# Kernel tuning notes

Hardware: AMD Instinct MI355X
Metric: run time of the kernel (lower is better)

The kernel has to match this reference:

```python
import jax, jax.numpy as jnp
import numpy as np

B, N, F, C, L = 2, 2048, 64, 64, 4

def setup_inputs() -> dict:
    key = jax.random.key(0)
    k1, k2, k3, k4, k5 = jax.random.split(key, 5)
    V = jax.random.normal(k1, (B, N, F), dtype=jnp.float32)
    A = jax.random.uniform(k2, (B, N, N, L), dtype=jnp.float32)
    # xavier-normal-ish scale for w1; plain normals for w2/w3
    w1 = jax.random.normal(k3, (F, C), dtype=jnp.float32) * jnp.sqrt(2.0 / (F + C))
    w2 = jax.random.normal(k4, (F * L, C), dtype=jnp.float32) * 0.05
    w3 = jax.random.normal(k5, (F * L, C), dtype=jnp.float32) * 0.05
    return {"V": V, "A": A, "w1": w1, "w2": w2, "w3": w3}

def reference(V, A, w1, w2, w3):
    b, n, _, l = A.shape
    f = V.shape[-1]
    # term1: plain linear embedding (no bias, no act)
    term1 = jnp.matmul(V, w1)                                   # B,N,C
    # term2: per-edge-type degree weighting of self features
    deg = jnp.sum(A, axis=2)                                    # B,N,L  (sum over neighbors j)
    dv = (deg[..., None] * V[:, :, None, :]).reshape(b, n, l * f)  # B,N,L*F
    term2 = jnp.matmul(dv, w2)                                  # B,N,C
    # term3: neighbor aggregation per edge type
    agg = jnp.einsum('bijl,bjf->bilf', A, V).reshape(b, n, l * f)  # B,N,L*F
    term3 = jnp.matmul(agg, w3)                                 # B,N,C
    return jax.nn.sigmoid(term1 + term2 - term3)
```

## Files before the change

### kernel.cpp

```cpp
#include <hip/hip_runtime.h>

#define B_ 2
#define N_ 2048
#define F_ 64
#define C_ 64
#define L_ 4
#define SK 4
#define NJ (N_ / SK)
#define TSTEPS (NJ / 32)
#define PJ 40

typedef _Float16 half8 __attribute__((ext_vector_type(8)));
typedef _Float16 half2 __attribute__((ext_vector_type(2)));
typedef float floatx4 __attribute__((ext_vector_type(4)));

__global__ __launch_bounds__(256) void k0_transpose(const float* __restrict__ V,
                                                    _Float16* __restrict__ Vth) {
    __shared__ float tile[64][65];
    const int b  = blockIdx.x >> 5;
    const int j0 = (blockIdx.x & 31) * 64;
    const int tid = threadIdx.x;

    const floatx4* V4 = (const floatx4*)(V + ((size_t)(b * N_ + j0)) * F_);
#pragma unroll
    for (int s = 0; s < 4; ++s) {
        int g = tid + 256 * s;
        int jl = g >> 4;
        int fq = g & 15;
        floatx4 v = V4[jl * 16 + fq];
        tile[jl][fq * 4 + 0] = v.x;
        tile[jl][fq * 4 + 1] = v.y;
        tile[jl][fq * 4 + 2] = v.z;
        tile[jl][fq * 4 + 3] = v.w;
    }
    __syncthreads();

    const int f = tid >> 2;
    const int jb = (tid & 3) * 16;
    _Float16* dh = Vth + ((size_t)(b * F_ + f)) * N_ + j0 + jb;
#pragma unroll
    for (int u = 0; u < 16; u += 4) {
        half2 h01 = {(_Float16)tile[jb + u + 0][f], (_Float16)tile[jb + u + 1][f]};
        half2 h23 = {(_Float16)tile[jb + u + 2][f], (_Float16)tile[jb + u + 3][f]};
        *(half2*)(dh + u + 0) = h01;
        *(half2*)(dh + u + 2) = h23;
    }
}

__global__ __launch_bounds__(256, 4) void k1_agg(const float* __restrict__ A,
                                                 const _Float16* __restrict__ Vth,
                                                 float* __restrict__ aggT,
                                                 float* __restrict__ degT) {
    __shared__ _Float16 lds[2 * 4 * 16 * PJ];

    const int bid = blockIdx.x;
    const int b   = bid >> 9;
    const int rem = bid & 511;
    const int i0  = (rem >> 2) * 16;
    const int p   = rem & 3;
    const int tid  = threadIdx.x;
    const int w    = tid >> 6;
    const int lane = tid & 63;
    const int m    = lane & 15;
    const int q    = lane >> 4;

    const int i_s = tid >> 4;
    const int jp  = tid & 15;

    const floatx4* Abase = (const floatx4*)A + ((size_t)(b * N_ + i0 + i_s)) * N_ + p * NJ;
    const _Float16* Vrow = Vth + ((size_t)b * F_) * N_ + p * NJ;

    floatx4 acc0 = {0,0,0,0}, acc1 = {0,0,0,0}, acc2 = {0,0,0,0}, acc3 = {0,0,0,0};
    floatx4 accd = {0,0,0,0};

    half8 bones;
#pragma unroll
    for (int e = 0; e < 8; ++e) bones[e] = (m == 0) ? (_Float16)1.0f : (_Float16)0.0f;

    floatx4 a_cur0, a_cur1, a_nxt0, a_nxt1;
    half8 v_cur0, v_cur1, v_cur2, v_cur3, v_nxt0, v_nxt1, v_nxt2, v_nxt3;

#define LOAD_A(t, x0, x1) do { int jj = (t) * 32 + 2 * jp; x0 = Abase[jj]; x1 = Abase[jj + 1]; } while (0)
#define LOAD_V(t, v0, v1, v2, v3) do { int jj = (t) * 32 + q * 8;                                  \
        v0 = *(const half8*)(Vrow + (size_t)(0  + m) * N_ + jj);                                   \
        v1 = *(const half8*)(Vrow + (size_t)(16 + m) * N_ + jj);                                   \
        v2 = *(const half8*)(Vrow + (size_t)(32 + m) * N_ + jj);                                   \
        v3 = *(const half8*)(Vrow + (size_t)(48 + m) * N_ + jj); } while (0)

    LOAD_A(0, a_cur0, a_cur1);
    LOAD_V(0, v_cur0, v_cur1, v_cur2, v_cur3);
    LOAD_A(1, a_nxt0, a_nxt1);
    LOAD_V(1, v_nxt0, v_nxt1, v_nxt2, v_nxt3);

#pragma unroll 2
    for (int t = 0; t < TSTEPS; ++t) {
        const int buf = t & 1;
        _Float16* dst = lds + buf * (4 * 16 * PJ);
        {
            const float* c0 = (const float*)&a_cur0;
            const float* c1 = (const float*)&a_cur1;
#pragma unroll
            for (int l = 0; l < 4; ++l) {
                half2 h = {(_Float16)c0[l], (_Float16)c1[l]};
                *(half2*)(dst + (l * 16 + i_s) * PJ + 2 * jp) = h;
            }
        }
        __syncthreads();

        a_cur0 = a_nxt0; a_cur1 = a_nxt1;
        const int tn = (t + 2 < TSTEPS) ? (t + 2) : (TSTEPS - 1);
        LOAD_A(tn, a_nxt0, a_nxt1);

        half8 af = *(const half8*)(lds + buf * (4 * 16 * PJ) + (w * 16 + m) * PJ + q * 8);
        acc0 = __builtin_amdgcn_mfma_f32_16x16x32_f16(af, v_cur0, acc0, 0, 0, 0);
        acc1 = __builtin_amdgcn_mfma_f32_16x16x32_f16(af, v_cur1, acc1, 0, 0, 0);
        acc2 = __builtin_amdgcn_mfma_f32_16x16x32_f16(af, v_cur2, acc2, 0, 0, 0);
        acc3 = __builtin_amdgcn_mfma_f32_16x16x32_f16(af, v_cur3, acc3, 0, 0, 0);
        accd = __builtin_amdgcn_mfma_f32_16x16x32_f16(af, bones,  accd, 0, 0, 0);

        v_cur0 = v_nxt0; v_cur1 = v_nxt1; v_cur2 = v_nxt2; v_cur3 = v_nxt3;
        LOAD_V(tn, v_nxt0, v_nxt1, v_nxt2, v_nxt3);
    }
#undef LOAD_A
#undef LOAD_V

    float* aggb = aggT + ((size_t)(p * B_ + b)) * 256 * N_;
    const int ibase = i0 + q * 4;
    {
        int k = w * 64 + 0  + m; *(floatx4*)(aggb + (size_t)k * N_ + ibase) = acc0;
    }
    {
        int k = w * 64 + 16 + m; *(floatx4*)(aggb + (size_t)k * N_ + ibase) = acc1;
    }
    {
        int k = w * 64 + 32 + m; *(floatx4*)(aggb + (size_t)k * N_ + ibase) = acc2;
    }
    {
        int k = w * 64 + 48 + m; *(floatx4*)(aggb + (size_t)k * N_ + ibase) = acc3;
    }
    if (m == 0) {
        *(floatx4*)(degT + ((size_t)((p * B_ + b) * L_ + w)) * N_ + ibase) = accd;
    }
}

__global__ __launch_bounds__(256) void k2_out(const float* __restrict__ V,
                                              const float* __restrict__ degT,
                                              const float* __restrict__ aggT,
                                              const float* __restrict__ w1,
                                              const float* __restrict__ w2,
                                              const float* __restrict__ w3,
                                              float* __restrict__ out) {
    __shared__ float xsum[256][4];
    __shared__ float vt[4][64];
    __shared__ float dsum[4][4];

    const int raw = blockIdx.x;
    const int b   = raw >> 9;
    const int t9  = raw & 511;
    const int tile = ((t9 & 7) << 6) | (t9 >> 3);
    const int i0  = tile * 4;
    const int tid = threadIdx.x;

    {
        const int k = tid;
        const float* g = aggT + ((size_t)b * 256 + k) * N_ + i0;
        const size_t PS = (size_t)B_ * 256 * N_;
        floatx4 s = *(const floatx4*)(g);
        s += *(const floatx4*)(g + PS);
        s += *(const floatx4*)(g + 2 * PS);
        s += *(const floatx4*)(g + 3 * PS);
        *(floatx4*)&xsum[k][0] = s;
    }
    {
        const int il = tid >> 6, f = tid & 63;
        vt[il][f] = V[((size_t)(b * N_ + i0 + il)) * F_ + f];
    }
    if (tid < 16) {
        const int l = tid >> 2, il = tid & 3;
        float s = 0.0f;
#pragma unroll
        for (int p = 0; p < SK; ++p)
            s += degT[((size_t)((p * B_ + b) * L_ + l)) * N_ + i0 + il];
        dsum[l][il] = s;
    }
    __syncthreads();

    const int il = tid >> 6;
    const int c  = tid & 63;
    const float d0 = dsum[0][il], d1 = dsum[1][il], d2 = dsum[2][il], d3 = dsum[3][il];

    float acc = 0.0f;
#pragma unroll 4
    for (int f = 0; f < 64; ++f) {
        const float x = vt[il][f];
        acc += x        * w1[f * 64 + c];
        acc += (d0 * x) * w2[(0 * 64 + f) * 64 + c];
        acc += (d1 * x) * w2[(1 * 64 + f) * 64 + c];
        acc += (d2 * x) * w2[(2 * 64 + f) * 64 + c];
        acc += (d3 * x) * w2[(3 * 64 + f) * 64 + c];
    }
#pragma unroll 4
    for (int k = 0; k < 256; ++k) {
        acc -= xsum[k][il] * w3[k * 64 + c];
    }

    out[((size_t)(b * N_ + i0 + il)) * C_ + c] = 1.0f / (1.0f + __expf(-acc));
}

extern "C" void kernel_launch(void* const* d_in, const int* in_sizes, int n_in,
                              void* d_out, int out_size, void* d_ws, size_t ws_size,
                              hipStream_t stream) {
    const float* V  = (const float*)d_in[0];
    const float* A  = (const float*)d_in[1];
    const float* w1 = (const float*)d_in[2];
    const float* w2 = (const float*)d_in[3];
    const float* w3 = (const float*)d_in[4];
    float* out = (float*)d_out;

    char* ws = (char*)d_ws;
    float*    aggT = (float*)(ws);
    float*    degT = (float*)(ws + 16777216);
    _Float16* Vth  = (_Float16*)(ws + 17039360);

    hipLaunchKernelGGL(k0_transpose, dim3(B_ * (N_ / 64)), dim3(256), 0, stream, V, Vth);
    hipLaunchKernelGGL(k1_agg,       dim3(B_ * (N_ / 16) * SK), dim3(256), 0, stream,
                       A, Vth, aggT, degT);
    hipLaunchKernelGGL(k2_out,       dim3(B_ * (N_ / 4)), dim3(256), 0, stream,
                       V, degT, aggT, w1, w2, w3, out);
}
```

Baseline: 243.2 us.

## Load A directly into MFMA registers per wave, drop LDS staging, split-K by 8

```diff
diff --git a/kernel.cpp b/kernel.cpp
--- a/kernel.cpp
+++ b/kernel.cpp
@@ -5,10 +5,7 @@
 #define F_ 64
 #define C_ 64
 #define L_ 4
-#define SK 4
-#define NJ (N_ / SK)
-#define TSTEPS (NJ / 32)
-#define PJ 40
+#define SP 8
 
 typedef _Float16 half8 __attribute__((ext_vector_type(8)));
 typedef _Float16 half2 __attribute__((ext_vector_type(2)));
@@ -47,99 +44,90 @@
     }
 }
 
-__global__ __launch_bounds__(256, 4) void k1_agg(const float* __restrict__ A,
+__global__ __launch_bounds__(256, 2) void k1_agg(const float* __restrict__ A,
                                                  const _Float16* __restrict__ Vth,
                                                  float* __restrict__ aggT,
                                                  float* __restrict__ degT) {
-    __shared__ _Float16 lds[2 * 4 * 16 * PJ];
-
     const int bid = blockIdx.x;
-    const int b   = bid >> 9;
-    const int rem = bid & 511;
-    const int i0  = (rem >> 2) * 16;
-    const int p   = rem & 3;
+    const int b   = bid >> 8;
+    const int rem = bid & 255;
+    const int i0  = (rem >> 1) * 16;
+    const int h   = rem & 1;
     const int tid  = threadIdx.x;
     const int w    = tid >> 6;
     const int lane = tid & 63;
     const int m    = lane & 15;
     const int q    = lane >> 4;
-
-    const int i_s = tid >> 4;
-    const int jp  = tid & 15;
-
-    const floatx4* Abase = (const floatx4*)A + ((size_t)(b * N_ + i0 + i_s)) * N_ + p * NJ;
-    const _Float16* Vrow = Vth + ((size_t)b * F_) * N_ + p * NJ;
-
-    floatx4 acc0 = {0,0,0,0}, acc1 = {0,0,0,0}, acc2 = {0,0,0,0}, acc3 = {0,0,0,0};
-    floatx4 accd = {0,0,0,0};
+    const int p    = h * 4 + w;
+    const int jwin = p * 256;
+
+    const floatx4* Arow = (const floatx4*)(A + (((size_t)(b * N_ + i0 + m)) * N_ + jwin) * 4);
+    const _Float16* Vrow = Vth + ((size_t)b * F_) * N_ + jwin;
+
+    floatx4 acc[4][4];
+    floatx4 accd[4];
+#pragma unroll
+    for (int l = 0; l < 4; ++l) {
+        accd[l] = (floatx4){0, 0, 0, 0};
+#pragma unroll
+        for (int fc = 0; fc < 4; ++fc) acc[l][fc] = (floatx4){0, 0, 0, 0};
+    }
 
     half8 bones;
 #pragma unroll
     for (int e = 0; e < 8; ++e) bones[e] = (m == 0) ? (_Float16)1.0f : (_Float16)0.0f;
 
-    floatx4 a_cur0, a_cur1, a_nxt0, a_nxt1;
-    half8 v_cur0, v_cur1, v_cur2, v_cur3, v_nxt0, v_nxt1, v_nxt2, v_nxt3;
-
-#define LOAD_A(t, x0, x1) do { int jj = (t) * 32 + 2 * jp; x0 = Abase[jj]; x1 = Abase[jj + 1]; } while (0)
-#define LOAD_V(t, v0, v1, v2, v3) do { int jj = (t) * 32 + q * 8;                                  \
-        v0 = *(const half8*)(Vrow + (size_t)(0  + m) * N_ + jj);                                   \
-        v1 = *(const half8*)(Vrow + (size_t)(16 + m) * N_ + jj);                                   \
-        v2 = *(const half8*)(Vrow + (size_t)(32 + m) * N_ + jj);                                   \
-        v3 = *(const half8*)(Vrow + (size_t)(48 + m) * N_ + jj); } while (0)
-
-    LOAD_A(0, a_cur0, a_cur1);
-    LOAD_V(0, v_cur0, v_cur1, v_cur2, v_cur3);
-    LOAD_A(1, a_nxt0, a_nxt1);
-    LOAD_V(1, v_nxt0, v_nxt1, v_nxt2, v_nxt3);
+    half8 v_cur[4], v_nxt[4];
+#pragma unroll
+    for (int fc = 0; fc < 4; ++fc)
+        v_cur[fc] = *(const half8*)(Vrow + (size_t)(fc * 16 + m) * N_ + q * 8);
 
 #pragma unroll 2
-    for (int t = 0; t < TSTEPS; ++t) {
-        const int buf = t & 1;
-        _Float16* dst = lds + buf * (4 * 16 * PJ);
-        {
-            const float* c0 = (const float*)&a_cur0;
-            const float* c1 = (const float*)&a_cur1;
-#pragma unroll
-            for (int l = 0; l < 4; ++l) {
-                half2 h = {(_Float16)c0[l], (_Float16)c1[l]};
-                *(half2*)(dst + (l * 16 + i_s) * PJ + 2 * jp) = h;
-            }
+    for (int t = 0; t < 8; ++t) {
+        floatx4 a[8];
+        const int jb = t * 32 + q * 8;
+#pragma unroll
+        for (int e = 0; e < 8; ++e) a[e] = Arow[jb + e];
+
+        const int tn = (t < 7) ? t + 1 : 7;
+        const int jn = tn * 32 + q * 8;
+#pragma unroll
+        for (int fc = 0; fc < 4; ++fc)
+            v_nxt[fc] = *(const half8*)(Vrow + (size_t)(fc * 16 + m) * N_ + jn);
+
+        half8 f[4];
+#pragma unroll
+        for (int l = 0; l < 4; ++l) {
+#pragma unroll
+            for (int e = 0; e < 8; ++e) f[l][e] = (_Float16)a[e][l];
         }
-        __syncthreads();
-
-        a_cur0 = a_nxt0; a_cur1 = a_nxt1;
-        const int tn = (t + 2 < TSTEPS) ? (t + 2) : (TSTEPS - 1);
-        LOAD_A(tn, a_nxt0, a_nxt1);
-
-        half8 af = *(const half8*)(lds + buf * (4 * 16 * PJ) + (w * 16 + m) * PJ + q * 8);
-        acc0 = __builtin_amdgcn_mfma_f32_16x16x32_f16(af, v_cur0, acc0, 0, 0, 0);
-        acc1 = __builtin_amdgcn_mfma_f32_16x16x32_f16(af, v_cur1, acc1, 0, 0, 0);
-        acc2 = __builtin_amdgcn_mfma_f32_16x16x32_f16(af, v_cur2, acc2, 0, 0, 0);
-        acc3 = __builtin_amdgcn_mfma_f32_16x16x32_f16(af, v_cur3, acc3, 0, 0, 0);
-        accd = __builtin_amdgcn_mfma_f32_16x16x32_f16(af, bones,  accd, 0, 0, 0);
-
-        v_cur0 = v_nxt0; v_cur1 = v_nxt1; v_cur2 = v_nxt2; v_cur3 = v_nxt3;
-        LOAD_V(tn, v_nxt0, v_nxt1, v_nxt2, v_nxt3);
-    }
-#undef LOAD_A
-#undef LOAD_V
+
+#pragma unroll
+        for (int l = 0; l < 4; ++l) {
+            acc[l][0] = __builtin_amdgcn_mfma_f32_16x16x32_f16(f[l], v_cur[0], acc[l][0], 0, 0, 0);
+            acc[l][1] = __builtin_amdgcn_mfma_f32_16x16x32_f16(f[l], v_cur[1], acc[l][1], 0, 0, 0);
+            acc[l][2] = __builtin_amdgcn_mfma_f32_16x16x32_f16(f[l], v_cur[2], acc[l][2], 0, 0, 0);
+            acc[l][3] = __builtin_amdgcn_mfma_f32_16x16x32_f16(f[l], v_cur[3], acc[l][3], 0, 0, 0);
+            accd[l]   = __builtin_amdgcn_mfma_f32_16x16x32_f16(f[l], bones,    accd[l],   0, 0, 0);
+        }
+#pragma unroll
+        for (int fc = 0; fc < 4; ++fc) v_cur[fc] = v_nxt[fc];
+    }
 
     float* aggb = aggT + ((size_t)(p * B_ + b)) * 256 * N_;
     const int ibase = i0 + q * 4;
-    {
-        int k = w * 64 + 0  + m; *(floatx4*)(aggb + (size_t)k * N_ + ibase) = acc0;
-    }
-    {
-        int k = w * 64 + 16 + m; *(floatx4*)(aggb + (size_t)k * N_ + ibase) = acc1;
-    }
-    {
-        int k = w * 64 + 32 + m; *(floatx4*)(aggb + (size_t)k * N_ + ibase) = acc2;
-    }
-    {
-        int k = w * 64 + 48 + m; *(floatx4*)(aggb + (size_t)k * N_ + ibase) = acc3;
+#pragma unroll
+    for (int l = 0; l < 4; ++l) {
+#pragma unroll
+        for (int fc = 0; fc < 4; ++fc) {
+            const int k = l * 64 + fc * 16 + m;
+            *(floatx4*)(aggb + (size_t)k * N_ + ibase) = acc[l][fc];
+        }
     }
     if (m == 0) {
-        *(floatx4*)(degT + ((size_t)((p * B_ + b) * L_ + w)) * N_ + ibase) = accd;
+#pragma unroll
+        for (int l = 0; l < 4; ++l)
+            *(floatx4*)(degT + ((size_t)((p * B_ + b) * L_ + l)) * N_ + ibase) = accd[l];
     }
 }
 
@@ -166,9 +154,8 @@
         const float* g = aggT + ((size_t)b * 256 + k) * N_ + i0;
         const size_t PS = (size_t)B_ * 256 * N_;
         floatx4 s = *(const floatx4*)(g);
-        s += *(const floatx4*)(g + PS);
-        s += *(const floatx4*)(g + 2 * PS);
-        s += *(const floatx4*)(g + 3 * PS);
+#pragma unroll
+        for (int pp = 1; pp < SP; ++pp) s += *(const floatx4*)(g + pp * PS);
         *(floatx4*)&xsum[k][0] = s;
     }
     {
@@ -179,8 +166,8 @@
         const int l = tid >> 2, il = tid & 3;
         float s = 0.0f;
 #pragma unroll
-        for (int p = 0; p < SK; ++p)
-            s += degT[((size_t)((p * B_ + b) * L_ + l)) * N_ + i0 + il];
+        for (int pp = 0; pp < SP; ++pp)
+            s += degT[((size_t)((pp * B_ + b) * L_ + l)) * N_ + i0 + il];
         dsum[l][il] = s;
     }
     __syncthreads();
@@ -219,11 +206,11 @@
 
     char* ws = (char*)d_ws;
     float*    aggT = (float*)(ws);
-    float*    degT = (float*)(ws + 16777216);
-    _Float16* Vth  = (_Float16*)(ws + 17039360);
+    float*    degT = (float*)(ws + 33554432);
+    _Float16* Vth  = (_Float16*)(ws + 34078720);
 
     hipLaunchKernelGGL(k0_transpose, dim3(B_ * (N_ / 64)), dim3(256), 0, stream, V, Vth);
-    hipLaunchKernelGGL(k1_agg,       dim3(B_ * (N_ / 16) * SK), dim3(256), 0, stream,
+    hipLaunchKernelGGL(k1_agg,       dim3(B_ * (N_ / 16) * 2), dim3(256), 0, stream,
                        A, Vth, aggT, degT);
     hipLaunchKernelGGL(k2_out,       dim3(B_ * (N_ / 4)), dim3(256), 0, stream,
                        V, degT, aggT, w1, w2, w3, out);
```

Measured after the change: 258.6 us. 6.3% more time.
